# Optimization experiments

Hardware: AMD Instinct MI355X
Metric: run time of the kernel (lower is better)

The kernel has to match this reference:

```python
import jax, jax.numpy as jnp
import numpy as np

C = 256  # in_channels
B, N = 8, 2048


def setup_inputs() -> dict:
    key = jax.random.key(0)
    ks = jax.random.split(key, 9)
    s = 1.0 / np.sqrt(C)  # conv1d default init scale (approx)
    return {
        "x": jax.random.normal(ks[0], (B, C, N), jnp.float32),
        "wq": jax.random.normal(ks[1], (C, C), jnp.float32) * s,
        "bq": jax.random.normal(ks[2], (C,), jnp.float32) * s,
        "wk": jax.random.normal(ks[3], (C, C), jnp.float32) * s,
        "bk": jax.random.normal(ks[4], (C,), jnp.float32) * s,
        "wv": jax.random.normal(ks[5], (C, C), jnp.float32) * s,
        "bv": jax.random.normal(ks[6], (C,), jnp.float32) * s,
        "wo": jax.random.normal(ks[7], (C, C), jnp.float32) * s,
        "bo": jax.random.normal(ks[8], (C,), jnp.float32) * s,
    }


def reference(x, wq, bq, wk, bk, wv, bv, wo, bo):
    # 1x1 Conv1d == channel-wise linear: [C_out,C_in] x [B,C_in,N] -> [B,C_out,N]
    proj = lambda w, b, t: jnp.einsum('ci,bin->bcn', w, t) + b[None, :, None]
    q = proj(wq, bq, x)
    k = proj(wk, bk, x)
    v = proj(wv, bv, x)
    norm = 1.0 / (x.shape[1] ** 0.5)
    # scores: w[b,n,m] = sum_c q[b,c,n] k[b,c,m]
    w = jnp.einsum('bcn,bcm->bnm', q, k) * norm
    w = jax.nn.softmax(w, axis=2)
    # attn output: sum_m v[b,c,m] w[b,n,m] -> [B,C,N]
    av = jnp.einsum('bcm,bnm->bcn', v, w)
    out = proj(wo, bo, av)
    return x + out
```

## Files before the change

### kernel.cpp

```cpp
#include <hip/hip_runtime.h>
#include <hip/hip_bf16.h>

#define CCH 256
#define NSEQ 2048
#define BATCH 8

typedef __hip_bfloat16 bf16;
typedef short s8v __attribute__((ext_vector_type(8)));
typedef float f4v __attribute__((ext_vector_type(4)));
typedef float f16v __attribute__((ext_vector_type(16)));

struct __align__(8) bf16x4 { bf16 v[4]; };

__device__ __forceinline__ float b2f(bf16 h) { return __bfloat162float(h); }
__device__ __forceinline__ bf16 f2b(float f) { return __float2bfloat16(f); }

#define MFMA16(a, b, c) __builtin_amdgcn_mfma_f32_16x16x32_bf16((a), (b), (c), 0, 0, 0)
#define MFMA32(a, b, c) __builtin_amdgcn_mfma_f32_32x32x16_bf16((a), (b), (c), 0, 0, 0)

__device__ __forceinline__ void gload_lds16(const bf16* g, bf16* l) {
    __builtin_amdgcn_global_load_lds(
        (const __attribute__((address_space(1))) unsigned int*)(g),
        (__attribute__((address_space(3))) unsigned int*)(l), 16, 0, 0);
}

__global__ __launch_bounds__(256) void prepw_kernel(
    const float* __restrict__ wq, const float* __restrict__ wk,
    const float* __restrict__ wv, const float* __restrict__ wo,
    bf16* __restrict__ wqb, bf16* __restrict__ wkb,
    bf16* __restrict__ wvb, bf16* __restrict__ wob)
{
    int base = (blockIdx.x * 256 + threadIdx.x) * 8;
    int mat = base >> 16, off = base & 65535;
    const float* s = (mat == 0) ? wq : (mat == 1) ? wk : (mat == 2) ? wv : wo;
    bf16* d = (mat == 0) ? wqb : (mat == 1) ? wkb : (mat == 2) ? wvb : wob;
    int doff = (mat == 3) ? off : (off ^ (((off >> 8) & 7) << 3));
    bf16 tmp[8];
    #pragma unroll
    for (int j = 0; j < 8; ++j) tmp[j] = f2b(s[off + j]);
    *(s8v*)&d[doff] = *(const s8v*)tmp;
}

__global__ __launch_bounds__(512, 4) void qkvprep_kernel(
    const float* __restrict__ x,
    const bf16* __restrict__ Wq, const bf16* __restrict__ Wk,
    const bf16* __restrict__ Wv,
    const float* __restrict__ bq, const float* __restrict__ bk,
    const float* __restrict__ bv,
    bf16* __restrict__ qTt, bf16* __restrict__ kTt, bf16* __restrict__ Vt)
{
    __shared__ bf16 xs[64][260];
    __shared__ bf16 wbuf[2][2][4096];

    const int tile = blockIdx.x;
    const int flat0 = tile * 64;
    const int phase = blockIdx.y;
    const int b = flat0 >> 11, nn = flat0 & 2047;
    const int tid = threadIdx.x;
    const int w = tid >> 6, lane = tid & 63;
    const int l15 = lane & 15, quad = lane >> 4;
    const int ng = w & 3;
    const int ch = w >> 2;
    const float* xb = x + (size_t)b * CCH * NSEQ;

    bf16* qt = qTt + (size_t)tile * 16384;
    bf16* kt = kTt + (size_t)tile * 16384;
    bf16* Vtb = Vt + (size_t)b * CCH * NSEQ;

    auto chunk_ptr = [&](int j) -> const bf16* {
        if (phase == 0)
            return (j < 8) ? Wq + (size_t)(ch * 8 + j) * 4096
                           : Wk + (size_t)(ch * 4 + (j - 8)) * 4096;
        else
            return (j < 8) ? Wv + (size_t)(ch * 8 + j) * 4096
                           : Wk + (size_t)(8 + ch * 4 + (j - 8)) * 4096;
    };
    auto stage = [&](int j, int par) {
        const bf16* src = chunk_ptr(j);
        bf16* dst = &wbuf[ch][par][0];
        int seg = (w & 3) * 2;
        gload_lds16(src + (seg + 0) * 512 + lane * 8, dst + (seg + 0) * 512);
        gload_lds16(src + (seg + 1) * 512 + lane * 8, dst + (seg + 1) * 512);
    };

    stage(0, 0);
    #pragma unroll
    for (int i = 0; i < 8; ++i) {
        int f4i = i * 512 + tid;
        int c = f4i >> 4, nq = f4i & 15;
        float4 v4 = *(const float4*)&xb[(size_t)c * NSEQ + nn + nq * 4];
        xs[nq * 4 + 0][c] = f2b(v4.x);
        xs[nq * 4 + 1][c] = f2b(v4.y);
        xs[nq * 4 + 2][c] = f2b(v4.z);
        xs[nq * 4 + 3][c] = f2b(v4.w);
    }
    __syncthreads();

    s8v xf[8];
    #pragma unroll
    for (int t = 0; t < 8; ++t)
        xf[t] = *(const s8v*)&xs[ng * 16 + l15][t * 32 + quad * 8];

    int par = 0;
    #pragma unroll
    for (int j = 0; j < 12; ++j) {
        if (j < 11) stage(j + 1, par ^ 1);

        const char* wb = (const char*)&wbuf[ch][par][0];
        s8v wf[8];
        #pragma unroll
        for (int t = 0; t < 8; ++t)
            wf[t] = *(const s8v*)(wb + l15 * 512 +
                                  ((t * 64 + quad * 16) ^ ((l15 & 7) << 4)));

        if (phase == 0 || j >= 8) {
            f4v a0 = {}, a1 = {};
            #pragma unroll
            for (int t = 0; t < 4; ++t) {
                a0 = MFMA16(wf[t], xf[t], a0);
                a1 = MFMA16(wf[t + 4], xf[t + 4], a1);
            }
            const bool isq = (phase == 0) && (j < 8);
            const int cs = (phase == 0)
                ? (j < 8 ? ch * 8 + j : ch * 4 + (j - 8))
                : (8 + ch * 4 + (j - 8));
            const float* bm = isq ? bq : bk;
            bf16* ot = isq ? qt : kt;
            const float sc = isq ? 0.0625f : 1.0f;
            float4 bb4 = *(const float4*)&bm[cs * 16 + quad * 4];
            float bbr[4] = { bb4.x, bb4.y, bb4.z, bb4.w };
            bf16x4 pk;
            #pragma unroll
            for (int r = 0; r < 4; ++r)
                pk.v[r] = f2b((a0[r] + a1[r] + bbr[r]) * sc);
            int nl = ng * 16 + l15;
            *(bf16x4*)&ot[(cs * 2 + (quad >> 1)) * 512 + nl * 8 + (quad & 1) * 4] = pk;
        } else {
            f4v a0 = {}, a1 = {};
            #pragma unroll
            for (int t = 0; t < 4; ++t) {
                a0 = MFMA16(xf[t], wf[t], a0);
                a1 = MFMA16(xf[t + 4], wf[t + 4], a1);
            }
            const int cs = ch * 8 + j;
            int c = cs * 16 + l15;
            float bb = bv[c];
            bf16x4 pk;
            #pragma unroll
            for (int r = 0; r < 4; ++r)
                pk.v[r] = f2b(a0[r] + a1[r] + bb);
            const int m16 = (nn >> 4) + ng;
            size_t e0 = ((size_t)m16 * 256 + c) * 16 + (quad >> 1) * 8 + (quad & 1) * 4;
            *(bf16x4*)&Vtb[e0] = pk;
        }
        __syncthreads();
        par ^= 1;
    }
}

__global__ __launch_bounds__(256, 2) void flash_kernel(
    const bf16* __restrict__ qTt, const bf16* __restrict__ kTt,
    const bf16* __restrict__ Vt, bf16* __restrict__ Opart,
    float* __restrict__ lpart)
{
    __shared__ bf16 Kc[16384];
    __shared__ bf16 Ps[64][68];
    __shared__ float l_s[2][64];

    const int b = blockIdx.x, nt = blockIdx.y, ms = blockIdx.z;
    const int tid = threadIdx.x;
    const int W = tid >> 6, lane = tid & 63;
    const int l31 = lane & 31, h = lane >> 5;
    const int ng = W >> 1, mg = W & 1;
    const int mb = ms * 16;
    const bf16* Vtb = Vt + (size_t)b * CCH * NSEQ;

    s8v qf[16];
    {
        const bf16* qt = qTt + (size_t)(b * 32 + nt) * 16384;
        #pragma unroll
        for (int t = 0; t < 16; ++t)
            qf[t] = *(const s8v*)&qt[(t * 2 + h) * 512 + (ng * 32 + l31) * 8];
    }
    const bf16* vbase = Vtb + (size_t)(W * 64 + l31) * 16 + h * 8;

    f16v O[2][2] = {};
    float lsum = 0.f;

    auto stageK = [&](int a) {
        const bf16* kt = kTt + (size_t)(b * 32 + a) * 16384;
        #pragma unroll
        for (int i = 0; i < 8; ++i) {
            int ch = W * 8 + i;
            gload_lds16(kt + ch * 512 + lane * 8, &Kc[ch * 512]);
        }
    };

    stageK(mb);
    __syncthreads();

    for (int mt = 0; mt < 16; ++mt) {
        s8v vf[2][4];
        #pragma unroll
        for (int ks = 0; ks < 4; ++ks)
            #pragma unroll
            for (int cr = 0; cr < 2; ++cr)
                vf[cr][ks] = *(const s8v*)(vbase
                    + (size_t)((mb + mt) * 4 + ks) * 4096 + cr * 512);

        f16v S0 = {}, S1 = {};
        __builtin_amdgcn_s_setprio(1);
        #pragma unroll
        for (int t = 0; t < 8; ++t) {
            s8v kf0 = *(const s8v*)&Kc[(t * 2 + h) * 512 + (mg * 32 + l31) * 8];
            s8v kf1 = *(const s8v*)&Kc[((t + 8) * 2 + h) * 512 + (mg * 32 + l31) * 8];
            S0 = MFMA32(kf0, qf[t], S0);
            S1 = MFMA32(kf1, qf[t + 8], S1);
        }
        __builtin_amdgcn_s_setprio(0);
        #pragma unroll
        for (int q = 0; q < 4; ++q) {
            bf16x4 pk;
            #pragma unroll
            for (int r = 0; r < 4; ++r) {
                float e = __expf(fminf(S0[q * 4 + r] + S1[q * 4 + r], 60.f));
                lsum += e;
                pk.v[r] = f2b(e);
            }
            *(bf16x4*)&Ps[ng * 32 + l31][mg * 32 + q * 8 + h * 4] = pk;
        }
        __syncthreads();

        if (mt < 15) stageK(mb + mt + 1);

        __builtin_amdgcn_s_setprio(1);
        #pragma unroll
        for (int ks = 0; ks < 4; ++ks) {
            s8v pf0 = *(const s8v*)&Ps[l31][ks * 16 + h * 8];
            s8v pf1 = *(const s8v*)&Ps[32 + l31][ks * 16 + h * 8];
            O[0][0] = MFMA32(vf[0][ks], pf0, O[0][0]);
            O[0][1] = MFMA32(vf[0][ks], pf1, O[0][1]);
            O[1][0] = MFMA32(vf[1][ks], pf0, O[1][0]);
            O[1][1] = MFMA32(vf[1][ks], pf1, O[1][1]);
        }
        __builtin_amdgcn_s_setprio(0);
        __syncthreads();
    }

    {
        float s = lsum + __shfl_xor(lsum, 32);
        if (h == 0) l_s[mg][ng * 32 + l31] = s;
    }
    __syncthreads();
    const size_t pb = (size_t)(b * 32 + nt) * 2 + ms;
    if (tid < 64) lpart[pb * 64 + tid] = l_s[0][tid] + l_s[1][tid];

    bf16* Ob = Opart + pb * 16384;
    #pragma unroll
    for (int cr = 0; cr < 2; ++cr)
        #pragma unroll
        for (int g2 = 0; g2 < 2; ++g2) {
            int n = g2 * 32 + l31;
            #pragma unroll
            for (int q2 = 0; q2 < 4; ++q2) {
                bf16x4 pk;
                #pragma unroll
                for (int j = 0; j < 4; ++j) pk.v[j] = f2b(O[cr][g2][q2 * 4 + j]);
                int c = W * 64 + cr * 32 + q2 * 8 + 4 * h;
                *(bf16x4*)&Ob[(size_t)n * 256 + c] = pk;
            }
        }
}

__global__ __launch_bounds__(512, 4) void outproj_kernel(
    const bf16* __restrict__ Opart, const float* __restrict__ lpart,
    const bf16* __restrict__ Wob, const float* __restrict__ bo,
    const float* __restrict__ x, float* __restrict__ out)
{
    __shared__ bf16 avs[64][260];
    __shared__ float ils[64];

    const int bx = blockIdx.x;
    const int flat0 = bx * 64;
    const int c0 = blockIdx.y * 128;
    const int tid = threadIdx.x;
    const int w = tid >> 6, lane = tid & 63;
    const int l15 = lane & 15, quad = lane >> 4;

    if (tid < 64)
        ils[tid] = 1.f / (lpart[(size_t)(bx * 2) * 64 + tid]
                        + lpart[(size_t)(bx * 2 + 1) * 64 + tid]);
    __syncthreads();

    const bf16x4* O0 = (const bf16x4*)(Opart + (size_t)(bx * 2) * 16384);
    const bf16x4* O1 = O0 + 4096;
    #pragma unroll
    for (int i = 0; i < 8; ++i) {
        int u = i * 512 + tid;
        int n = u >> 6;
        bf16x4 a = O0[u], bb = O1[u];
        float il = ils[n];
        bf16x4 o;
        #pragma unroll
        for (int t = 0; t < 4; ++t)
            o.v[t] = f2b((b2f(a.v[t]) + b2f(bb.v[t])) * il);
        *(bf16x4*)&avs[n][(u & 63) * 4] = o;
    }
    __syncthreads();

    const int bidx = flat0 >> 11, nn = flat0 & 2047;
    const size_t base = (size_t)bidx * CCH * NSEQ;
    const int cg = c0 + w * 16;

    s8v af[8];
    #pragma unroll
    for (int t = 0; t < 8; ++t)
        af[t] = *(const s8v*)&Wob[(size_t)(cg + l15) * CCH + t * 32 + quad * 8];

    f4v O[4] = {};
    #pragma unroll
    for (int nt = 0; nt < 4; ++nt)
        #pragma unroll
        for (int t = 0; t < 8; ++t) {
            s8v br = *(const s8v*)&avs[nt * 16 + l15][t * 32 + quad * 8];
            O[nt] = MFMA16(af[t], br, O[nt]);
        }
    #pragma unroll
    for (int r = 0; r < 4; ++r) {
        int c = cg + quad * 4 + r;
        float bb = bo[c];
        #pragma unroll
        for (int nt = 0; nt < 4; ++nt) {
            size_t idx = base + (size_t)c * NSEQ + nn + nt * 16 + l15;
            out[idx] = O[nt][r] + bb + x[idx];
        }
    }
}

extern "C" void kernel_launch(void* const* d_in, const int* in_sizes, int n_in,
                              void* d_out, int out_size, void* d_ws, size_t ws_size,
                              hipStream_t stream) {
    (void)in_sizes; (void)n_in; (void)out_size; (void)ws_size;
    const float* x  = (const float*)d_in[0];
    const float* wq = (const float*)d_in[1];
    const float* bq = (const float*)d_in[2];
    const float* wk = (const float*)d_in[3];
    const float* bk = (const float*)d_in[4];
    const float* wv = (const float*)d_in[5];
    const float* bv = (const float*)d_in[6];
    const float* wo = (const float*)d_in[7];
    const float* bo = (const float*)d_in[8];
    float* out = (float*)d_out;

    const size_t T = (size_t)BATCH * CCH * NSEQ;
    bf16* qTt  = (bf16*)d_ws;
    bf16* kTt  = qTt + T;
    bf16* Vt   = kTt + T;
    bf16* wqb  = Vt + T;
    bf16* wkb  = wqb + 65536;
    bf16* wvb  = wkb + 65536;
    bf16* wob  = wvb + 65536;
    float* lpart = (float*)(wob + 65536);
    bf16* Opart  = (bf16*)(lpart + 32768);

    prepw_kernel<<<128, 256, 0, stream>>>(wq, wk, wv, wo, wqb, wkb, wvb, wob);
    qkvprep_kernel<<<dim3(256, 2), 512, 0, stream>>>(
        x, wqb, wkb, wvb, bq, bk, bv, qTt, kTt, Vt);
    flash_kernel<<<dim3(8, 32, 2), 256, 0, stream>>>(qTt, kTt, Vt, Opart, lpart);
    outproj_kernel<<<dim3(256, 2), 512, 0, stream>>>(Opart, lpart, wob, bo, x, out);
}
```

Before: 154.7 us.

## Split flash attention key range three ways and widen partial output stores

The key dimension of the flash kernel is now split into three uneven chunks instead of two, giving 768 blocks. Occupancy is raised to three blocks per CU, and the outproj kernel now sums three partials. The V fragment loads move after the score MFMAs to lower register pressure. Partial outputs are written as 16-byte nontemporal stores after a lane shuffle. The cost is more partial-buffer traffic and extra reduction work in outproj, with possible register spills at the higher occupancy.

Result: slower. 266.0 us (+71.9%).

```diff
diff --git a/kernel.cpp b/kernel.cpp
--- a/kernel.cpp
+++ b/kernel.cpp
@@ -9,6 +9,7 @@
 typedef short s8v __attribute__((ext_vector_type(8)));
 typedef float f4v __attribute__((ext_vector_type(4)));
 typedef float f16v __attribute__((ext_vector_type(16)));
+typedef int i4v __attribute__((ext_vector_type(4)));
 
 struct __align__(8) bf16x4 { bf16 v[4]; };
 
@@ -158,7 +159,7 @@
     }
 }
 
-__global__ __launch_bounds__(256, 2) void flash_kernel(
+__global__ __launch_bounds__(256, 3) void flash_kernel(
     const bf16* __restrict__ qTt, const bf16* __restrict__ kTt,
     const bf16* __restrict__ Vt, bf16* __restrict__ Opart,
     float* __restrict__ lpart)
@@ -172,7 +173,7 @@
     const int W = tid >> 6, lane = tid & 63;
     const int l31 = lane & 31, h = lane >> 5;
     const int ng = W >> 1, mg = W & 1;
-    const int mb = ms * 16;
+    const int a0 = (ms * 32) / 3, a1 = ((ms + 1) * 32) / 3;
     const bf16* Vtb = Vt + (size_t)b * CCH * NSEQ;
 
     s8v qf[16];
@@ -196,18 +197,10 @@
         }
     };
 
-    stageK(mb);
-    __syncthreads();
-
-    for (int mt = 0; mt < 16; ++mt) {
-        s8v vf[2][4];
-        #pragma unroll
-        for (int ks = 0; ks < 4; ++ks)
-            #pragma unroll
-            for (int cr = 0; cr < 2; ++cr)
-                vf[cr][ks] = *(const s8v*)(vbase
-                    + (size_t)((mb + mt) * 4 + ks) * 4096 + cr * 512);
-
+    stageK(a0);
+    __syncthreads();
+
+    for (int a = a0; a < a1; ++a) {
         f16v S0 = {}, S1 = {};
         __builtin_amdgcn_s_setprio(1);
         #pragma unroll
@@ -218,6 +211,13 @@
             S1 = MFMA32(kf1, qf[t + 8], S1);
         }
         __builtin_amdgcn_s_setprio(0);
+        s8v vf[2][4];
+        #pragma unroll
+        for (int ks = 0; ks < 4; ++ks)
+            #pragma unroll
+            for (int cr = 0; cr < 2; ++cr)
+                vf[cr][ks] = *(const s8v*)(vbase
+                    + (size_t)(a * 4 + ks) * 4096 + cr * 512);
         #pragma unroll
         for (int q = 0; q < 4; ++q) {
             bf16x4 pk;
@@ -231,7 +231,7 @@
         }
         __syncthreads();
 
-        if (mt < 15) stageK(mb + mt + 1);
+        if (a + 1 < a1) stageK(a + 1);
 
         __builtin_amdgcn_s_setprio(1);
         #pragma unroll
@@ -252,8 +252,10 @@
         if (h == 0) l_s[mg][ng * 32 + l31] = s;
     }
     __syncthreads();
-    const size_t pb = (size_t)(b * 32 + nt) * 2 + ms;
-    if (tid < 64) lpart[pb * 64 + tid] = l_s[0][tid] + l_s[1][tid];
+    const size_t pb = (size_t)(b * 32 + nt) * 3 + ms;
+    if (tid < 64)
+        __builtin_nontemporal_store(l_s[0][tid] + l_s[1][tid],
+                                    &lpart[pb * 64 + tid]);
 
     bf16* Ob = Opart + pb * 16384;
     #pragma unroll
@@ -261,13 +263,27 @@
         #pragma unroll
         for (int g2 = 0; g2 < 2; ++g2) {
             int n = g2 * 32 + l31;
+            uint2 mp[4];
             #pragma unroll
             for (int q2 = 0; q2 < 4; ++q2) {
                 bf16x4 pk;
                 #pragma unroll
                 for (int j = 0; j < 4; ++j) pk.v[j] = f2b(O[cr][g2][q2 * 4 + j]);
-                int c = W * 64 + cr * 32 + q2 * 8 + 4 * h;
-                *(bf16x4*)&Ob[(size_t)n * 256 + c] = pk;
+                mp[q2] = *(uint2*)&pk;
+            }
+            #pragma unroll
+            for (int q2 = 0; q2 < 4; ++q2) {
+                uint2 op;
+                op.x = __shfl_xor(mp[q2].x, 32);
+                op.y = __shfl_xor(mp[q2].y, 32);
+                if ((q2 >> 1) == h) {
+                    uint2 lo = h ? op : mp[q2];
+                    uint2 hi = h ? mp[q2] : op;
+                    i4v val = { (int)lo.x, (int)lo.y, (int)hi.x, (int)hi.y };
+                    int c0 = W * 64 + cr * 32 + q2 * 8;
+                    __builtin_nontemporal_store(
+                        val, (i4v*)&Ob[(size_t)n * 256 + c0]);
+                }
             }
         }
 }
@@ -288,22 +304,24 @@
     const int l15 = lane & 15, quad = lane >> 4;
 
     if (tid < 64)
-        ils[tid] = 1.f / (lpart[(size_t)(bx * 2) * 64 + tid]
-                        + lpart[(size_t)(bx * 2 + 1) * 64 + tid]);
-    __syncthreads();
-
-    const bf16x4* O0 = (const bf16x4*)(Opart + (size_t)(bx * 2) * 16384);
+        ils[tid] = 1.f / (lpart[(size_t)(bx * 3) * 64 + tid]
+                        + lpart[(size_t)(bx * 3 + 1) * 64 + tid]
+                        + lpart[(size_t)(bx * 3 + 2) * 64 + tid]);
+    __syncthreads();
+
+    const bf16x4* O0 = (const bf16x4*)(Opart + (size_t)(bx * 3) * 16384);
     const bf16x4* O1 = O0 + 4096;
+    const bf16x4* O2 = O1 + 4096;
     #pragma unroll
     for (int i = 0; i < 8; ++i) {
         int u = i * 512 + tid;
         int n = u >> 6;
-        bf16x4 a = O0[u], bb = O1[u];
+        bf16x4 a = O0[u], bb = O1[u], cc = O2[u];
         float il = ils[n];
         bf16x4 o;
         #pragma unroll
         for (int t = 0; t < 4; ++t)
-            o.v[t] = f2b((b2f(a.v[t]) + b2f(bb.v[t])) * il);
+            o.v[t] = f2b((b2f(a.v[t]) + b2f(bb.v[t]) + b2f(cc.v[t])) * il);
         *(bf16x4*)&avs[n][(u & 63) * 4] = o;
     }
     __syncthreads();
@@ -361,11 +379,11 @@
     bf16* wvb  = wkb + 65536;
     bf16* wob  = wvb + 65536;
     float* lpart = (float*)(wob + 65536);
-    bf16* Opart  = (bf16*)(lpart + 32768);
+    bf16* Opart  = (bf16*)(lpart + 768 * 64);
 
     prepw_kernel<<<128, 256, 0, stream>>>(wq, wk, wv, wo, wqb, wkb, wvb, wob);
     qkvprep_kernel<<<dim3(256, 2), 512, 0, stream>>>(
         x, wqb, wkb, wvb, bq, bk, bv, qTt, kTt, Vt);
-    flash_kernel<<<dim3(8, 32, 2), 256, 0, stream>>>(qTt, kTt, Vt, Opart, lpart);
+    flash_kernel<<<dim3(8, 32, 3), 256, 0, stream>>>(qTt, kTt, Vt, Opart, lpart);
     outproj_kernel<<<dim3(256, 2), 512, 0, stream>>>(Opart, lpart, wob, bo, x, out);
 }
```
